# Kernel optimization log

Measured on AMD Instinct MI355X. Metric: run time of the kernel, lower is better.

The kernel has to match this reference:

```python
import jax, jax.numpy as jnp
import numpy as np

B, T, C, N = 2, 2048, 4096, 4096

def setup_inputs() -> dict:
    key = jax.random.key(0)
    k1, k2, k3, k4 = jax.random.split(key, 4)
    y = jax.random.normal(k1, (B, T, C), dtype=jnp.float32)
    # quantized weight: uint8 codes in [0,255], stored/used as float after upcast
    weight = jnp.round(jax.random.uniform(k2, (C, N), dtype=jnp.float32) * 255.0)
    rng = jax.random.uniform(k3, (1, 1, C), dtype=jnp.float32) * 0.01  # per-input-channel scale
    offset = jax.random.normal(k4, (C,), dtype=jnp.float32) * 0.01    # per-input-channel offset
    return {"y": y, "weight": weight, "rng": rng, "offset": offset}

def reference(y, weight, rng, offset):
    # yv = y.reshape(-1,C) @ offset -> [B,T,1] correction term
    yv = jnp.einsum('btc,c->bt', y, offset)[..., None]
    # (y * range) @ weight  (dequantized GEMM) + correction
    out = jnp.einsum('btc,cn->btn', y * rng, weight) + yv
    return out
```

## Files before the change

kernel.cpp:

```cpp
#include <hip/hip_runtime.h>

typedef unsigned short u16;
typedef unsigned int u32;
typedef unsigned char u8;
typedef signed char i8;

typedef int i32x4 __attribute__((ext_vector_type(4)));

__device__ inline void gld16(const i8* g, i8* l) {
    __builtin_amdgcn_global_load_lds((const __attribute__((address_space(1))) void*)g,
                                     (__attribute__((address_space(3))) void*)l,
                                     16, 0, 0);
}

__global__ __launch_bounds__(256) void prep_kernel(const float* __restrict__ y,
                                                   const float* __restrict__ rng,
                                                   const float* __restrict__ off,
                                                   const float* __restrict__ w,
                                                   uint4* __restrict__ qy,
                                                   uint4* __restrict__ wq,
                                                   float* __restrict__ sp,
                                                   float* __restrict__ tv) {
    __shared__ i8 tile[64][68];
    __shared__ float ra[4], rs1[4], rs2[4];
    const int tid = threadIdx.x;

    if (blockIdx.x < 4096) {
        const int row = blockIdx.x;
        const float* yr = y + (size_t)row * 4096;
        const int base = tid * 16;

        float ysr[16];
        float amax = 0.0f, s1 = 0.0f, s2 = 0.0f;
        #pragma unroll
        for (int ii = 0; ii < 4; ++ii) {
            float4 v = *(const float4*)&yr[base + ii * 4];
            float4 g = *(const float4*)&rng[base + ii * 4];
            float4 o = *(const float4*)&off[base + ii * 4];
            float p0 = v.x * g.x, p1 = v.y * g.y, p2 = v.z * g.z, p3 = v.w * g.w;
            ysr[ii * 4 + 0] = p0; ysr[ii * 4 + 1] = p1;
            ysr[ii * 4 + 2] = p2; ysr[ii * 4 + 3] = p3;
            s1 += p0 + p1 + p2 + p3;
            s2 += v.x * o.x + v.y * o.y + v.z * o.z + v.w * o.w;
            amax = fmaxf(amax, fmaxf(fmaxf(fabsf(p0), fabsf(p1)), fmaxf(fabsf(p2), fabsf(p3))));
        }
        #pragma unroll
        for (int d = 32; d > 0; d >>= 1) {
            amax = fmaxf(amax, __shfl_down(amax, d));
            s1 += __shfl_down(s1, d);
            s2 += __shfl_down(s2, d);
        }
        const int wv = tid >> 6;
        if ((tid & 63) == 0) { ra[wv] = amax; rs1[wv] = s1; rs2[wv] = s2; }
        __syncthreads();
        const float sm = fmaxf(fmaxf(ra[0], ra[1]), fmaxf(ra[2], ra[3]));
        const float inv = sm > 0.0f ? 127.0f / sm : 0.0f;

        u32 d[4];
        #pragma unroll
        for (int g = 0; g < 4; ++g) {
            u32 b0 = (u8)(i8)(int)rintf(ysr[g * 4 + 0] * inv);
            u32 b1 = (u8)(i8)(int)rintf(ysr[g * 4 + 1] * inv);
            u32 b2 = (u8)(i8)(int)rintf(ysr[g * 4 + 2] * inv);
            u32 b3 = (u8)(i8)(int)rintf(ysr[g * 4 + 3] * inv);
            d[g] = b0 | (b1 << 8) | (b2 << 16) | (b3 << 24);
        }
        const int j = (tid & 7) ^ (row & 7);
        qy[(size_t)row * 256 + (tid >> 3) * 8 + j] = make_uint4(d[0], d[1], d[2], d[3]);
        if (tid == 0) {
            sp[row] = sm / 127.0f;
            tv[row] = 128.0f * (rs1[0] + rs1[1] + rs1[2] + rs1[3])
                            + (rs2[0] + rs2[1] + rs2[2] + rs2[3]);
        }
    } else {
        const int bid = blockIdx.x - 4096;
        const int n0 = (bid & 63) * 64;
        const int k0 = (bid >> 6) * 64;
        const int c4 = tid & 15;
        const int r0 = tid >> 4;
        #pragma unroll
        for (int i = 0; i < 4; ++i) {
            int kk = r0 + i * 16;
            float4 v = *(const float4*)&w[(size_t)(k0 + kk) * 4096 + n0 + c4 * 4];
            u32 b0 = (u8)(i8)((int)v.x - 128);
            u32 b1 = (u8)(i8)((int)v.y - 128);
            u32 b2 = (u8)(i8)((int)v.z - 128);
            u32 b3 = (u8)(i8)((int)v.w - 128);
            *(u32*)&tile[kk][c4 * 4] = b0 | (b1 << 8) | (b2 << 16) | (b3 << 24);
        }
        __syncthreads();
        const int nl = tid >> 2;
        const int ci = tid & 3;
        const int l = ((k0 >> 4) & 7) + ci;
        const int j = l ^ ((n0 + nl) & 7);
        u32 d[4];
        #pragma unroll
        for (int g = 0; g < 4; ++g) {
            int kl = ci * 16 + g * 4;
            d[g] = (u32)(u8)tile[kl + 0][nl] | ((u32)(u8)tile[kl + 1][nl] << 8)
                 | ((u32)(u8)tile[kl + 2][nl] << 16) | ((u32)(u8)tile[kl + 3][nl] << 24);
        }
        wq[(size_t)(n0 + nl) * 256 + (k0 >> 7) * 8 + j] = make_uint4(d[0], d[1], d[2], d[3]);
    }
}

__global__ __launch_bounds__(512, 2) void gemm_kernel(const i8* __restrict__ qy,
                                                      const i8* __restrict__ wq,
                                                      const float* __restrict__ sp,
                                                      const float* __restrict__ tv,
                                                      float* __restrict__ out) {
    __shared__ i8 As[2][256 * 128];
    __shared__ i8 Bs[2][256 * 128];

    const int bid = blockIdx.x;
    const int xcd = bid & 7;
    const int jj = bid >> 3;
    const int bn = (xcd * 2 + (jj & 1)) * 256;
    const int bm = (jj >> 1) * 256;

    const int tid = (int)threadIdx.x;
    const int lane = tid & 63;
    const int wv = tid >> 6;
    const int wm = (wv >> 2) * 128;
    const int wn = (wv & 3) * 64;
    const int r = lane & 15;
    const int q = lane >> 4;
    const int col0 = (q ^ (r & 7)) << 4;

    const int offA0 = (wm + r) * 128 + col0;
    const int offB0 = (wn + r) * 128 + col0;
    const int offA1 = offA0 ^ 64;
    const int offB1 = offB0 ^ 64;

    const int rsub = lane >> 3;
    const int jsub = lane & 7;
    const i8* aP0 = qy + (size_t)(bm + wv * 8 + rsub) * 4096 + jsub * 16;
    const i8* bP0 = wq + (size_t)(bn + (wv >> 2) * 64 + (wv & 3) * 8 + rsub) * 4096 + jsub * 16;
    const int lAo = wv * 1024 + lane * 16;
    const int lBo = (wv >> 2) * 8192 + (wv & 3) * 1024 + lane * 16;

    size_t koff = 0;

#define STAGE_A(WB, H) do {                                                   \
        gld16(aP0 + koff + (size_t)((H) * 64) * 4096,       &As[WB][lAo + (H) * 8192]);          \
        gld16(aP0 + koff + (size_t)((H) * 64 + 128) * 4096, &As[WB][lAo + (H) * 8192 + 16384]);  \
    } while (0)
#define STAGE_B(WB, H) do {                                                   \
        gld16(bP0 + koff + (size_t)((H) * 32) * 4096,       &Bs[WB][lBo + (H) * 4096]);          \
        gld16(bP0 + koff + (size_t)((H) * 32 + 128) * 4096, &Bs[WB][lBo + (H) * 4096 + 16384]);  \
    } while (0)

    i32x4 acc[8][4] = {};
    i32x4 a[4][2], aa[4][2], b[4][2];

    STAGE_A(0, 0); STAGE_B(0, 0); STAGE_B(0, 1); STAGE_A(0, 1);
    koff = 128;
    asm volatile("s_waitcnt vmcnt(0)" ::: "memory");
    __builtin_amdgcn_s_barrier();

#define SB __builtin_amdgcn_sched_barrier(0)

#define RD_A4K(RB, MB, DST, KS)                                               \
    _Pragma("unroll")                                                         \
    for (int mi = 0; mi < 4; ++mi) {                                          \
        DST[mi][KS] = *(const i32x4*)&As[RB][((KS) ? offA1 : offA0) + (MB + mi) * 2048]; \
    }
#define RD_B4K(RB, KS)                                                        \
    _Pragma("unroll")                                                         \
    for (int ni = 0; ni < 4; ++ni) {                                          \
        b[ni][KS] = *(const i32x4*)&Bs[RB][((KS) ? offB1 : offB0) + ni * 2048]; \
    }
#define MM16(MB, SRC, KS)                                                     \
    _Pragma("unroll")                                                         \
    for (int mi = 0; mi < 4; ++mi) {                                          \
        _Pragma("unroll")                                                     \
        for (int ni = 0; ni < 4; ++ni) {                                      \
            acc[MB + mi][ni] = __builtin_amdgcn_mfma_i32_16x16x64_i8(         \
                SRC[mi][KS], b[ni][KS], acc[MB + mi][ni], 0, 0, 0);           \
        }                                                                     \
    }

#define KTILE(RB, WB, PF)                                                     \
    do {                                                                      \
                                            \
        RD_A4K(RB, 0, a, 0); RD_B4K(RB, 0); SB;                               \
                                            \
        RD_A4K(RB, 0, a, 1); RD_B4K(RB, 1); SB;                               \
          \
        if (PF) { STAGE_A(WB, 0); STAGE_B(WB, 0); STAGE_B(WB, 1); STAGE_A(WB, 1); } \
        SB;                                                                   \
        __builtin_amdgcn_s_setprio(1);                                        \
        asm volatile("s_waitcnt lgkmcnt(8)" ::: "memory"); SB;   \
        MM16(0, a, 0); SB;                                                    \
                        \
        RD_A4K(RB, 4, aa, 0); SB;                                             \
        RD_A4K(RB, 4, aa, 1); SB;                                             \
        asm volatile("s_waitcnt lgkmcnt(8)" ::: "memory"); SB;   \
        MM16(0, a, 1); SB;                                                    \
        asm volatile("s_waitcnt lgkmcnt(4)" ::: "memory"); SB;   \
        MM16(4, aa, 0); SB;                                                   \
        asm volatile("s_waitcnt lgkmcnt(0)" ::: "memory"); SB;   \
        MM16(4, aa, 1);                                                       \
        __builtin_amdgcn_s_setprio(0);                                        \
        asm volatile("s_waitcnt vmcnt(0)" ::: "memory");                      \
        __builtin_amdgcn_s_barrier();                                         \
        koff += 128;                                                          \
    } while (0)

    #pragma unroll 1
    for (int t = 0; t < 15; ++t) {
        KTILE(0, 1, 1);
        KTILE(1, 0, 1);
    }
    KTILE(0, 1, 1);
    KTILE(1, 0, 0);

#undef KTILE
#undef MM16
#undef RD_B4K
#undef RD_A4K
#undef SB
#undef STAGE_B
#undef STAGE_A

    #pragma unroll
    for (int mi = 0; mi < 8; ++mi) {
        #pragma unroll
        for (int rr = 0; rr < 4; ++rr) {
            const int gm = bm + wm + mi * 16 + q * 4 + rr;
            const float sc = sp[gm];
            const float tt = tv[gm];
            #pragma unroll
            for (int ni = 0; ni < 4; ++ni) {
                const int gn = bn + wn + ni * 16 + r;
                out[(size_t)gm * 4096 + gn] = sc * (float)acc[mi][ni][rr] + tt;
            }
        }
    }
}

extern "C" void kernel_launch(void* const* d_in, const int* in_sizes, int n_in,
                              void* d_out, int out_size, void* d_ws, size_t ws_size,
                              hipStream_t stream) {
    const float* y   = (const float*)d_in[0];
    const float* w   = (const float*)d_in[1];
    const float* rng = (const float*)d_in[2];
    const float* off = (const float*)d_in[3];
    float* out = (float*)d_out;

    i8* qy = (i8*)d_ws;
    i8* wq = qy + (size_t)4096 * 4096;
    float* sp = (float*)(wq + (size_t)4096 * 4096);
    float* tv = sp + 4096;

    prep_kernel<<<8192, 256, 0, stream>>>(y, rng, off, w, (uint4*)qy, (uint4*)wq, sp, tv);
    gemm_kernel<<<256, 512, 0, stream>>>(qy, wq, sp, tv, out);
}
```

Before: 230.5 us.

## Load B operand directly from global into registers, bypassing LDS

Drops the shared-memory staging buffer for the weight tile. Each wave now loads its B fragments straight from global memory into a double-buffered register set (b0/b1), prefetched one k-tile ahead, with vmcnt waits adjusted. This removes LDS traffic and LDS capacity for B, which could raise occupancy, at the cost of more registers and more global-load requests. Global loads are no longer shared across waves, so the same B data is fetched by more than one wave.

After: 242.2 us. +5.1%, slower.

```diff
diff --git a/kernel.cpp b/kernel.cpp
--- a/kernel.cpp
+++ b/kernel.cpp
@@ -110,7 +110,6 @@
                                                       const float* __restrict__ tv,
                                                       float* __restrict__ out) {
     __shared__ i8 As[2][256 * 128];
-    __shared__ i8 Bs[2][256 * 128];
 
     const int bid = blockIdx.x;
     const int xcd = bid & 7;
@@ -128,16 +127,15 @@
     const int col0 = (q ^ (r & 7)) << 4;
 
     const int offA0 = (wm + r) * 128 + col0;
-    const int offB0 = (wn + r) * 128 + col0;
     const int offA1 = offA0 ^ 64;
-    const int offB1 = offB0 ^ 64;
+
+    const i8* bQ0 = wq + (size_t)(bn + wn + r) * 4096 + col0;
+    const i8* bQ1 = wq + (size_t)(bn + wn + r) * 4096 + (col0 ^ 64);
 
     const int rsub = lane >> 3;
     const int jsub = lane & 7;
     const i8* aP0 = qy + (size_t)(bm + wv * 8 + rsub) * 4096 + jsub * 16;
-    const i8* bP0 = wq + (size_t)(bn + (wv >> 2) * 64 + (wv & 3) * 8 + rsub) * 4096 + jsub * 16;
     const int lAo = wv * 1024 + lane * 16;
-    const int lBo = (wv >> 2) * 8192 + (wv & 3) * 1024 + lane * 16;
 
     size_t koff = 0;
 
@@ -145,82 +143,82 @@
         gld16(aP0 + koff + (size_t)((H) * 64) * 4096,       &As[WB][lAo + (H) * 8192]);          \
         gld16(aP0 + koff + (size_t)((H) * 64 + 128) * 4096, &As[WB][lAo + (H) * 8192 + 16384]);  \
     } while (0)
-#define STAGE_B(WB, H) do {                                                   \
-        gld16(bP0 + koff + (size_t)((H) * 32) * 4096,       &Bs[WB][lBo + (H) * 4096]);          \
-        gld16(bP0 + koff + (size_t)((H) * 32 + 128) * 4096, &Bs[WB][lBo + (H) * 4096 + 16384]);  \
+
+#define LOAD_B(DST) do {                                                      \
+        _Pragma("unroll")                                                     \
+        for (int ni = 0; ni < 4; ++ni) {                                      \
+            DST[ni][0] = *(const i32x4*)(bQ0 + koff + ni * 65536);            \
+            DST[ni][1] = *(const i32x4*)(bQ1 + koff + ni * 65536);            \
+        }                                                                     \
     } while (0)
 
     i32x4 acc[8][4] = {};
-    i32x4 a[4][2], aa[4][2], b[4][2];
-
-    STAGE_A(0, 0); STAGE_B(0, 0); STAGE_B(0, 1); STAGE_A(0, 1);
+    i32x4 a[4][2];
+    i32x4 b0[4][2], b1[4][2];
+
+    STAGE_A(0, 0); STAGE_A(0, 1);
+    LOAD_B(b0);
     koff = 128;
-    asm volatile("s_waitcnt vmcnt(0)" ::: "memory");
+    asm volatile("s_waitcnt vmcnt(8)" ::: "memory");
     __builtin_amdgcn_s_barrier();
 
 #define SB __builtin_amdgcn_sched_barrier(0)
 
-#define RD_A4K(RB, MB, DST, KS)                                               \
+#define RD_A4K(RB, MB, KS)                                                    \
     _Pragma("unroll")                                                         \
     for (int mi = 0; mi < 4; ++mi) {                                          \
-        DST[mi][KS] = *(const i32x4*)&As[RB][((KS) ? offA1 : offA0) + (MB + mi) * 2048]; \
-    }
-#define RD_B4K(RB, KS)                                                        \
-    _Pragma("unroll")                                                         \
-    for (int ni = 0; ni < 4; ++ni) {                                          \
-        b[ni][KS] = *(const i32x4*)&Bs[RB][((KS) ? offB1 : offB0) + ni * 2048]; \
-    }
-#define MM16(MB, SRC, KS)                                                     \
+        a[mi][KS] = *(const i32x4*)&As[RB][((KS) ? offA1 : offA0) + (MB + mi) * 2048]; \
+    }
+#define MM16(MB, BC, KS)                                                      \
     _Pragma("unroll")                                                         \
     for (int mi = 0; mi < 4; ++mi) {                                          \
         _Pragma("unroll")                                                     \
         for (int ni = 0; ni < 4; ++ni) {                                      \
             acc[MB + mi][ni] = __builtin_amdgcn_mfma_i32_16x16x64_i8(         \
-                SRC[mi][KS], b[ni][KS], acc[MB + mi][ni], 0, 0, 0);           \
+                a[mi][KS], BC[ni][KS], acc[MB + mi][ni], 0, 0, 0);            \
         }                                                                     \
     }
 
-#define KTILE(RB, WB, PF)                                                     \
+#define KTILE(RB, WB, BC, BNX, PF)                                            \
     do {                                                                      \
-                                            \
-        RD_A4K(RB, 0, a, 0); RD_B4K(RB, 0); SB;                               \
-                                            \
-        RD_A4K(RB, 0, a, 1); RD_B4K(RB, 1); SB;                               \
-          \
-        if (PF) { STAGE_A(WB, 0); STAGE_B(WB, 0); STAGE_B(WB, 1); STAGE_A(WB, 1); } \
-        SB;                                                                   \
+        if (PF) { STAGE_A(WB, 0); STAGE_A(WB, 1); } SB;                       \
+        if (PF) { LOAD_B(BNX); } SB;                                          \
+                                                           \
+        RD_A4K(RB, 0, 0); SB;                                                 \
+        RD_A4K(RB, 0, 1); SB;                                                 \
         __builtin_amdgcn_s_setprio(1);                                        \
-        asm volatile("s_waitcnt lgkmcnt(8)" ::: "memory"); SB;   \
-        MM16(0, a, 0); SB;                                                    \
-                        \
-        RD_A4K(RB, 4, aa, 0); SB;                                             \
-        RD_A4K(RB, 4, aa, 1); SB;                                             \
-        asm volatile("s_waitcnt lgkmcnt(8)" ::: "memory"); SB;   \
-        MM16(0, a, 1); SB;                                                    \
-        asm volatile("s_waitcnt lgkmcnt(4)" ::: "memory"); SB;   \
-        MM16(4, aa, 0); SB;                                                   \
-        asm volatile("s_waitcnt lgkmcnt(0)" ::: "memory"); SB;   \
-        MM16(4, aa, 1);                                                       \
+        asm volatile("s_waitcnt lgkmcnt(4)" ::: "memory"); SB;                \
+        MM16(0, BC, 0); SB;                                                   \
+        asm volatile("s_waitcnt lgkmcnt(0)" ::: "memory"); SB;                \
+        MM16(0, BC, 1); SB;                                                   \
+                      \
+        RD_A4K(RB, 4, 0); SB;                                                 \
+        RD_A4K(RB, 4, 1); SB;                                                 \
+        asm volatile("s_waitcnt lgkmcnt(4)" ::: "memory"); SB;                \
+        MM16(4, BC, 0); SB;                                                   \
+        asm volatile("s_waitcnt lgkmcnt(0)" ::: "memory"); SB;                \
+        MM16(4, BC, 1);                                                       \
         __builtin_amdgcn_s_setprio(0);                                        \
-        asm volatile("s_waitcnt vmcnt(0)" ::: "memory");                      \
+                \
+        if (PF) asm volatile("s_waitcnt vmcnt(8)" ::: "memory");              \
+        else    asm volatile("s_waitcnt vmcnt(0)" ::: "memory");              \
         __builtin_amdgcn_s_barrier();                                         \
         koff += 128;                                                          \
     } while (0)
 
     #pragma unroll 1
     for (int t = 0; t < 15; ++t) {
-        KTILE(0, 1, 1);
-        KTILE(1, 0, 1);
-    }
-    KTILE(0, 1, 1);
-    KTILE(1, 0, 0);
+        KTILE(0, 1, b0, b1, 1);
+        KTILE(1, 0, b1, b0, 1);
+    }
+    KTILE(0, 1, b0, b1, 1);
+    KTILE(1, 0, b1, b0, 0);
 
 #undef KTILE
 #undef MM16
-#undef RD_B4K
 #undef RD_A4K
 #undef SB
-#undef STAGE_B
+#undef LOAD_B
 #undef STAGE_A
 
     #pragma unroll
```
